# Performance work log

Hardware: AMD Instinct MI355X
Metric: run time of the kernel (lower is better)

## Reference

```python
import jax, jax.numpy as jnp
import numpy as np

NUM_EMBEDDINGS = 512
EMBEDDING_DIM = 64
COMMITMENT_COST = 0.25


def setup_inputs() -> dict:
    key = jax.random.key(0)
    k1, k2 = jax.random.split(key)
    inputs = jax.random.normal(k1, (64, 32, 32, EMBEDDING_DIM), dtype=jnp.float32)
    # codebook initialized uniform(-1/K, 1/K) as in the torch module
    codebook = jax.random.uniform(
        k2, (NUM_EMBEDDINGS, EMBEDDING_DIM), dtype=jnp.float32,
        minval=-1.0 / NUM_EMBEDDINGS, maxval=1.0 / NUM_EMBEDDINGS)
    return {"inputs": inputs, "codebook": codebook}


def reference(inputs, codebook):
    D = codebook.shape[1]
    K = codebook.shape[0]
    flat = inputs.reshape(-1, D)  # [N, D]
    distances = (jnp.sum(flat * flat, axis=1, keepdims=True)
                 + jnp.sum(codebook * codebook, axis=1)
                 - 2.0 * jnp.matmul(flat, codebook.T))
    idx = jnp.argmin(distances, axis=1)  # [N]
    # direct gather == one-hot @ codebook
    quantized = codebook[idx].reshape(inputs.shape)
    e_latent_loss = jnp.mean((jax.lax.stop_gradient(quantized) - inputs) ** 2)
    q_latent_loss = jnp.mean((quantized - jax.lax.stop_gradient(inputs)) ** 2)
    loss = q_latent_loss + COMMITMENT_COST * e_latent_loss
    # straight-through estimator
    quantized_st = inputs + jax.lax.stop_gradient(quantized - inputs)
    # avg_probs = mean over N of one-hot encodings == normalized bincount
    counts = jnp.zeros((K,), dtype=jnp.float32).at[idx].add(1.0)
    avg_probs = counts / flat.shape[0]
    perplexity = jnp.exp(-jnp.sum(avg_probs * jnp.log(avg_probs + 1e-10)))
    return (quantized_st, loss, perplexity)
```

## Files before the change

kernel.cpp:

```cpp
#include <hip/hip_runtime.h>
#include <stdint.h>


#define VQ_N 65536
#define VQ_D 64
#define VQ_K 512
#define HIST_BLOCKS 32

typedef __attribute__((ext_vector_type(4))) float f32x4;
typedef __attribute__((ext_vector_type(8))) short bf16x8;

__device__ __forceinline__ unsigned short f2bf(float f) {
    unsigned b = __float_as_uint(f);
    return (unsigned short)((b + 0x7fffu + ((b >> 16) & 1u)) >> 16);
}

__device__ __forceinline__ void gld_lds16(const void* g, void* l) {
    __builtin_amdgcn_global_load_lds(
        (const __attribute__((address_space(1))) void*)g,
        (__attribute__((address_space(3))) void*)(uintptr_t)(
            (char*)l - (char*)nullptr),
        16, 0, 0);
}

__global__ __launch_bounds__(256) void vq_prep(const float* __restrict__ cb,
                                               unsigned short* __restrict__ Bfrag,
                                               float* __restrict__ sq_e) {
    int g = blockIdx.x * 256 + threadIdx.x;
    int lane = g & 63, kt = (g >> 6) & 1, ct = g >> 7;
    int col = ct * 16 + (lane & 15);
    int k0 = kt * 32 + (lane >> 4) * 8;
    const float4* p = reinterpret_cast<const float4*>(cb + (size_t)col * VQ_D + k0);
    float4 v0 = p[0], v1 = p[1];
    float vv[8] = {v0.x, v0.y, v0.z, v0.w, v1.x, v1.y, v1.z, v1.w};
    bf16x8 h;
#pragma unroll
    for (int j = 0; j < 8; ++j) h[j] = (short)f2bf(vv[j]);
    reinterpret_cast<bf16x8*>(Bfrag)[(size_t)(ct * 2 + kt) * 64 + lane] = h;

    if (g < VQ_K) {
        const float4* row = reinterpret_cast<const float4*>(cb + (size_t)g * VQ_D);
        float s = 0.0f;
#pragma unroll
        for (int i = 0; i < VQ_D / 4; ++i) {
            float4 v = row[i];
            s += v.x * v.x + v.y * v.y + v.z * v.z + v.w * v.w;
        }
        sq_e[g] = s;
    }
}

__global__ __launch_bounds__(256, 4) void vq_fused(const float* __restrict__ x,
                                                   const unsigned short* __restrict__ Bfrag,
                                                   const float* __restrict__ cb,
                                                   const float* __restrict__ sq_e,
                                                   float* __restrict__ out,
                                                   int* __restrict__ idx_out,
                                                   float* __restrict__ loss_part) {
    __shared__ unsigned short lds[16384];
    __shared__ float lds_se[VQ_K];
    __shared__ int sbestk[64];
    __shared__ float wsum[4];
    const bf16x8* ldsV = reinterpret_cast<const bf16x8*>(lds);

    int t = threadIdx.x;
    int w = t >> 6, l = t & 63;
    int lr = l & 15, lg = l >> 4;
    int rowbase = blockIdx.x * 64 + w * 16;

    lds_se[t] = sq_e[t];
    lds_se[t + 256] = sq_e[t + 256];

    bf16x8 Ah[2];
    float sq;
    {
        float part = 0.0f;
#pragma unroll
        for (int kt = 0; kt < 2; ++kt) {
            const float4* p = reinterpret_cast<const float4*>(
                x + (size_t)(rowbase + lr) * VQ_D + kt * 32 + lg * 8);
            float4 v0 = p[0], v1 = p[1];
            float vv[8] = {v0.x, v0.y, v0.z, v0.w, v1.x, v1.y, v1.z, v1.w};
            bf16x8 h;
#pragma unroll
            for (int j = 0; j < 8; ++j) {
                h[j] = (short)f2bf(-2.0f * vv[j]);
                part = fmaf(vv[j], vv[j], part);
            }
            Ah[kt] = h;
        }
        part += __shfl_xor(part, 16);
        part += __shfl_xor(part, 32);
        sq = part;
    }

    float bd[4];
    int bc[4];
#pragma unroll
    for (int j = 0; j < 4; ++j) {
        bd[j] = 3.4e38f;
        bc[j] = 0;
    }

    for (int c = 0; c < 2; ++c) {
        __syncthreads();
#pragma unroll
        for (int i = 0; i < 8; ++i) {
            int e = i * 256 + w * 64;
            gld_lds16(Bfrag + ((size_t)c * 2048 + e + l) * 8, (void*)&lds[e * 8]);
        }
        __syncthreads();

#pragma unroll
        for (int ct2 = 0; ct2 < 16; ++ct2) {
            int col = c * 256 + ct2 * 16 + lr;
            float se = lds_se[col];
            bf16x8 b0 = ldsV[ct2 * 128 + l];
            bf16x8 b1 = ldsV[ct2 * 128 + 64 + l];
            f32x4 a0 = {se, se, se, se};
            a0 = __builtin_amdgcn_mfma_f32_16x16x32_bf16(Ah[0], b0, a0, 0, 0, 0);
            a0 = __builtin_amdgcn_mfma_f32_16x16x32_bf16(Ah[1], b1, a0, 0, 0, 0);
#pragma unroll
            for (int j = 0; j < 4; ++j) {
                if (a0[j] < bd[j]) {
                    bd[j] = a0[j];
                    bc[j] = col;
                }
            }
        }
    }

    float dacc = 0.0f;
#pragma unroll
    for (int j = 0; j < 4; ++j) {
        float d = bd[j];
        int cc = bc[j];
#pragma unroll
        for (int off = 1; off <= 8; off <<= 1) {
            float od = __shfl_xor(d, off);
            int oc = __shfl_xor(cc, off);
            if (od < d || (od == d && oc < cc)) {
                d = od;
                cc = oc;
            }
        }
        if (lr == 0) {
            int rloc = w * 16 + lg * 4 + j;
            sbestk[rloc] = cc;
            idx_out[blockIdx.x * 64 + rloc] = cc;
            dacc += d;
        }
    }

    float contrib = dacc + (lg == 0 ? sq : 0.0f);
#pragma unroll
    for (int off = 32; off; off >>= 1) contrib += __shfl_down(contrib, off);
    if (l == 0) wsum[w] = contrib;
    __syncthreads();
    if (t == 0)
        loss_part[blockIdx.x] = (wsum[0] + wsum[1]) + (wsum[2] + wsum[3]);

    {
        int r = t >> 2, q = t & 3;
        int k = sbestk[r];
        const float4* src =
            reinterpret_cast<const float4*>(cb + (size_t)k * VQ_D + q * 16);
        float4* dst = reinterpret_cast<float4*>(
            out + ((size_t)blockIdx.x * 64 + r) * VQ_D + q * 16);
#pragma unroll
        for (int i = 0; i < 4; ++i) dst[i] = src[i];
    }
}

__global__ __launch_bounds__(256) void vq_hist(const int* __restrict__ idx,
                                               unsigned* __restrict__ partial) {
    __shared__ unsigned h[VQ_K];
    int t = threadIdx.x;
    h[t] = 0u;
    h[t + 256] = 0u;
    __syncthreads();
    int base = blockIdx.x * (VQ_N / HIST_BLOCKS) + t;
#pragma unroll
    for (int i = 0; i < VQ_N / HIST_BLOCKS / 256; ++i)
        atomicAdd(&h[idx[base + i * 256]], 1u);
    __syncthreads();
    partial[blockIdx.x * VQ_K + t] = h[t];
    partial[blockIdx.x * VQ_K + t + 256] = h[t + 256];
}

__global__ void vq_final(const unsigned* __restrict__ partial,
                         const float* __restrict__ loss_part,
                         float* __restrict__ out_tail) {
    int t = threadIdx.x;
    unsigned cnt = 0;
#pragma unroll
    for (int b = 0; b < HIST_BLOCKS; ++b) cnt += partial[b * VQ_K + t];
    float p = (float)cnt * (1.0f / (float)VQ_N);
    float term = p * logf(p + 1e-10f);
    float ls = loss_part[t] + loss_part[t + 512];
#pragma unroll
    for (int off = 32; off; off >>= 1) {
        term += __shfl_down(term, off);
        ls += __shfl_down(ls, off);
    }
    __shared__ float wsH[8], wsL[8];
    int wave = t >> 6, lane = t & 63;
    if (lane == 0) {
        wsH[wave] = term;
        wsL[wave] = ls;
    }
    __syncthreads();
    if (t == 0) {
        float H = 0.0f, L = 0.0f;
#pragma unroll
        for (int i = 0; i < 8; ++i) {
            H += wsH[i];
            L += wsL[i];
        }
        out_tail[0] = L * (1.25f / (float)(VQ_N * VQ_D));
        out_tail[1] = expf(-H);
    }
}

extern "C" void kernel_launch(void* const* d_in, const int* in_sizes, int n_in,
                              void* d_out, int out_size, void* d_ws, size_t ws_size,
                              hipStream_t stream) {
    const float* x = (const float*)d_in[0];
    const float* cb = (const float*)d_in[1];
    float* out = (float*)d_out;

    unsigned short* Bfrag = (unsigned short*)d_ws;
    float* sq_e = (float*)((char*)d_ws + (64 << 10));
    int* idx = (int*)((char*)d_ws + (66 << 10));
    float* loss_part = (float*)((char*)d_ws + (66 << 10) + VQ_N * 4);
    unsigned* partial = (unsigned*)((char*)loss_part + 4096);

    vq_prep<<<16, 256, 0, stream>>>(cb, Bfrag, sq_e);
    vq_fused<<<VQ_N / 64, 256, 0, stream>>>(x, Bfrag, cb, sq_e, out, idx, loss_part);
    vq_hist<<<HIST_BLOCKS, 256, 0, stream>>>(idx, partial);
    vq_final<<<1, 512, 0, stream>>>(partial, loss_part, out + (size_t)VQ_N * VQ_D);
}
```

Baseline: 32.58 us.

## Fuse codebook bf16 prep into main kernel with 128-row blocks

Removes the separate prep kernel. Each block now converts the whole fp32 codebook to bf16 MFMA fragments in LDS and computes the codebook squared norms itself. Blocks grow to 512 threads handling 128 rows, with the full 64KB codebook resident in LDS, so the two-chunk reload loop and its extra barriers go away. This saves a launch and a global round trip through the workspace. In exchange every block redoes the conversion and norm work from L2, and the larger LDS footprint lowers how many blocks fit per CU.

```diff
diff --git a/kernel.cpp b/kernel.cpp
--- a/kernel.cpp
+++ b/kernel.cpp
@@ -15,61 +15,21 @@
     return (unsigned short)((b + 0x7fffu + ((b >> 16) & 1u)) >> 16);
 }
 
-__device__ __forceinline__ void gld_lds16(const void* g, void* l) {
-    __builtin_amdgcn_global_load_lds(
-        (const __attribute__((address_space(1))) void*)g,
-        (__attribute__((address_space(3))) void*)(uintptr_t)(
-            (char*)l - (char*)nullptr),
-        16, 0, 0);
-}
-
-__global__ __launch_bounds__(256) void vq_prep(const float* __restrict__ cb,
-                                               unsigned short* __restrict__ Bfrag,
-                                               float* __restrict__ sq_e) {
-    int g = blockIdx.x * 256 + threadIdx.x;
-    int lane = g & 63, kt = (g >> 6) & 1, ct = g >> 7;
-    int col = ct * 16 + (lane & 15);
-    int k0 = kt * 32 + (lane >> 4) * 8;
-    const float4* p = reinterpret_cast<const float4*>(cb + (size_t)col * VQ_D + k0);
-    float4 v0 = p[0], v1 = p[1];
-    float vv[8] = {v0.x, v0.y, v0.z, v0.w, v1.x, v1.y, v1.z, v1.w};
-    bf16x8 h;
-#pragma unroll
-    for (int j = 0; j < 8; ++j) h[j] = (short)f2bf(vv[j]);
-    reinterpret_cast<bf16x8*>(Bfrag)[(size_t)(ct * 2 + kt) * 64 + lane] = h;
-
-    if (g < VQ_K) {
-        const float4* row = reinterpret_cast<const float4*>(cb + (size_t)g * VQ_D);
-        float s = 0.0f;
-#pragma unroll
-        for (int i = 0; i < VQ_D / 4; ++i) {
-            float4 v = row[i];
-            s += v.x * v.x + v.y * v.y + v.z * v.z + v.w * v.w;
-        }
-        sq_e[g] = s;
-    }
-}
-
-__global__ __launch_bounds__(256, 4) void vq_fused(const float* __restrict__ x,
-                                                   const unsigned short* __restrict__ Bfrag,
+__global__ __launch_bounds__(512, 4) void vq_fused(const float* __restrict__ x,
                                                    const float* __restrict__ cb,
-                                                   const float* __restrict__ sq_e,
                                                    float* __restrict__ out,
                                                    int* __restrict__ idx_out,
                                                    float* __restrict__ loss_part) {
-    __shared__ unsigned short lds[16384];
+    __shared__ unsigned short ldsB[32768];
     __shared__ float lds_se[VQ_K];
-    __shared__ int sbestk[64];
-    __shared__ float wsum[4];
-    const bf16x8* ldsV = reinterpret_cast<const bf16x8*>(lds);
+    __shared__ int sbestk[128];
+    __shared__ float wsum[8];
+    const bf16x8* ldsV = reinterpret_cast<const bf16x8*>(ldsB);
 
     int t = threadIdx.x;
     int w = t >> 6, l = t & 63;
     int lr = l & 15, lg = l >> 4;
-    int rowbase = blockIdx.x * 64 + w * 16;
-
-    lds_se[t] = sq_e[t];
-    lds_se[t + 256] = sq_e[t + 256];
+    int rowbase = blockIdx.x * 128 + w * 16;
 
     bf16x8 Ah[2];
     float sq;
@@ -94,6 +54,33 @@
         sq = part;
     }
 
+#pragma unroll
+    for (int i = 0; i < 8; ++i) {
+        int e = i * 512 + t;
+        int lane = e & 63, kt = (e >> 6) & 1, ct = e >> 7;
+        int col = ct * 16 + (lane & 15);
+        int k0 = kt * 32 + (lane >> 4) * 8;
+        const float4* p = reinterpret_cast<const float4*>(cb + col * VQ_D + k0);
+        float4 v0 = p[0], v1 = p[1];
+        float vv[8] = {v0.x, v0.y, v0.z, v0.w, v1.x, v1.y, v1.z, v1.w};
+        bf16x8 h;
+#pragma unroll
+        for (int j = 0; j < 8; ++j) h[j] = (short)f2bf(vv[j]);
+        reinterpret_cast<bf16x8*>(ldsB)[e] = h;
+    }
+    {
+        const float4* row = reinterpret_cast<const float4*>(cb + t * VQ_D);
+        float s = 0.0f;
+#pragma unroll
+        for (int i = 0; i < VQ_D / 4; ++i) {
+            float4 v = row[i];
+            s += v.x * v.x + v.y * v.y + v.z * v.z + v.w * v.w;
+        }
+        lds_se[t] = s;
+    }
+
+    __syncthreads();
+
     float bd[4];
     int bc[4];
 #pragma unroll
@@ -101,31 +88,20 @@
         bd[j] = 3.4e38f;
         bc[j] = 0;
     }
-
-    for (int c = 0; c < 2; ++c) {
-        __syncthreads();
-#pragma unroll
-        for (int i = 0; i < 8; ++i) {
-            int e = i * 256 + w * 64;
-            gld_lds16(Bfrag + ((size_t)c * 2048 + e + l) * 8, (void*)&lds[e * 8]);
-        }
-        __syncthreads();
-
-#pragma unroll
-        for (int ct2 = 0; ct2 < 16; ++ct2) {
-            int col = c * 256 + ct2 * 16 + lr;
-            float se = lds_se[col];
-            bf16x8 b0 = ldsV[ct2 * 128 + l];
-            bf16x8 b1 = ldsV[ct2 * 128 + 64 + l];
-            f32x4 a0 = {se, se, se, se};
-            a0 = __builtin_amdgcn_mfma_f32_16x16x32_bf16(Ah[0], b0, a0, 0, 0, 0);
-            a0 = __builtin_amdgcn_mfma_f32_16x16x32_bf16(Ah[1], b1, a0, 0, 0, 0);
-#pragma unroll
-            for (int j = 0; j < 4; ++j) {
-                if (a0[j] < bd[j]) {
-                    bd[j] = a0[j];
-                    bc[j] = col;
-                }
+#pragma unroll
+    for (int ct2 = 0; ct2 < 32; ++ct2) {
+        int col = ct2 * 16 + lr;
+        float se = lds_se[col];
+        bf16x8 b0 = ldsV[ct2 * 128 + l];
+        bf16x8 b1 = ldsV[ct2 * 128 + 64 + l];
+        f32x4 a0 = {se, se, se, se};
+        a0 = __builtin_amdgcn_mfma_f32_16x16x32_bf16(Ah[0], b0, a0, 0, 0, 0);
+        a0 = __builtin_amdgcn_mfma_f32_16x16x32_bf16(Ah[1], b1, a0, 0, 0, 0);
+#pragma unroll
+        for (int j = 0; j < 4; ++j) {
+            if (a0[j] < bd[j]) {
+                bd[j] = a0[j];
+                bc[j] = col;
             }
         }
     }
@@ -147,7 +123,7 @@
         if (lr == 0) {
             int rloc = w * 16 + lg * 4 + j;
             sbestk[rloc] = cc;
-            idx_out[blockIdx.x * 64 + rloc] = cc;
+            idx_out[blockIdx.x * 128 + rloc] = cc;
             dacc += d;
         }
     }
@@ -157,8 +133,12 @@
     for (int off = 32; off; off >>= 1) contrib += __shfl_down(contrib, off);
     if (l == 0) wsum[w] = contrib;
     __syncthreads();
-    if (t == 0)
-        loss_part[blockIdx.x] = (wsum[0] + wsum[1]) + (wsum[2] + wsum[3]);
+    if (t == 0) {
+        float s = 0.0f;
+#pragma unroll
+        for (int i = 0; i < 8; ++i) s += wsum[i];
+        loss_part[blockIdx.x] = s;
+    }
 
     {
         int r = t >> 2, q = t & 3;
@@ -166,7 +146,7 @@
         const float4* src =
             reinterpret_cast<const float4*>(cb + (size_t)k * VQ_D + q * 16);
         float4* dst = reinterpret_cast<float4*>(
-            out + ((size_t)blockIdx.x * 64 + r) * VQ_D + q * 16);
+            out + ((size_t)blockIdx.x * 128 + r) * VQ_D + q * 16);
 #pragma unroll
         for (int i = 0; i < 4; ++i) dst[i] = src[i];
     }
@@ -197,7 +177,7 @@
     for (int b = 0; b < HIST_BLOCKS; ++b) cnt += partial[b * VQ_K + t];
     float p = (float)cnt * (1.0f / (float)VQ_N);
     float term = p * logf(p + 1e-10f);
-    float ls = loss_part[t] + loss_part[t + 512];
+    float ls = loss_part[t];
 #pragma unroll
     for (int off = 32; off; off >>= 1) {
         term += __shfl_down(term, off);
@@ -229,14 +209,11 @@
     const float* cb = (const float*)d_in[1];
     float* out = (float*)d_out;
 
-    unsigned short* Bfrag = (unsigned short*)d_ws;
-    float* sq_e = (float*)((char*)d_ws + (64 << 10));
-    int* idx = (int*)((char*)d_ws + (66 << 10));
-    float* loss_part = (float*)((char*)d_ws + (66 << 10) + VQ_N * 4);
-    unsigned* partial = (unsigned*)((char*)loss_part + 4096);
-
-    vq_prep<<<16, 256, 0, stream>>>(cb, Bfrag, sq_e);
-    vq_fused<<<VQ_N / 64, 256, 0, stream>>>(x, Bfrag, cb, sq_e, out, idx, loss_part);
+    int* idx = (int*)d_ws;
+    float* loss_part = (float*)((char*)d_ws + (VQ_N * 4));
+    unsigned* partial = (unsigned*)((char*)loss_part + 2048);
+
+    vq_fused<<<VQ_N / 128, 512, 0, stream>>>(x, cb, out, idx, loss_part);
     vq_hist<<<HIST_BLOCKS, 256, 0, stream>>>(idx, partial);
     vq_final<<<1, 512, 0, stream>>>(partial, loss_part, out + (size_t)VQ_N * VQ_D);
 }
```

Measured after the change: 40.66 us. +24.8%, slower.
